# Kernel optimization log

Measured on AMD Instinct MI355X. Metric: run time of the kernel, lower is better.

The kernel has to match this reference:

```python
import jax, jax.numpy as jnp
import numpy as np

DIM = 768
HEADS = 12

def setup_inputs() -> dict:
    key = jax.random.key(0)
    ks = jax.random.split(key, 5)
    x = jax.random.normal(ks[0], (8, 1024, DIM), dtype=jnp.float32)
    s = 1.0 / np.sqrt(DIM)
    W_qkv = jax.random.normal(ks[1], (DIM, 3 * DIM), dtype=jnp.float32) * s
    b_qkv = jax.random.normal(ks[2], (3 * DIM,), dtype=jnp.float32) * 0.01
    W_proj = jax.random.normal(ks[3], (DIM, DIM), dtype=jnp.float32) * s
    b_proj = jax.random.normal(ks[4], (DIM,), dtype=jnp.float32) * 0.01
    return {"x": x, "W_qkv": W_qkv, "b_qkv": b_qkv, "W_proj": W_proj, "b_proj": b_proj}

def reference(x, W_qkv, b_qkv, W_proj, b_proj):
    B, T, D = x.shape
    H = HEADS
    hd = D // H
    scale = hd ** -0.5
    qkv = x @ W_qkv + b_qkv                      # [B,T,3D]
    qkv = qkv.reshape(B, T, 3, H, hd)
    q, k, v = jnp.moveaxis(qkv, 2, 0)            # each [B,T,H,hd]
    q = jnp.transpose(q, (0, 2, 1, 3))           # [B,H,T,hd]
    k = jnp.transpose(k, (0, 2, 1, 3))
    v = jnp.transpose(v, (0, 2, 1, 3))
    attn = jnp.einsum('bhqd,bhkd->bhqk', q, k) * scale
    attn = jax.nn.softmax(attn, axis=-1)
    y = jnp.einsum('bhqk,bhkd->bhqd', attn, v)   # [B,H,T,hd]
    y = jnp.transpose(y, (0, 2, 1, 3)).reshape(B, T, D)
    return y @ W_proj + b_proj
```

## Files before the change

kernel.cpp:

```cpp
#include <hip/hip_runtime.h>

typedef unsigned short u16;
typedef __attribute__((ext_vector_type(8))) short short8;
typedef __attribute__((ext_vector_type(4))) short short4v;
typedef __attribute__((ext_vector_type(2))) int int2v;
typedef __attribute__((ext_vector_type(4))) float f32x4;

#define DIM   768
#define HEADS 12
#define HD    64
#define BATCH 8
#define SEQ   1024
#define MTOK  (BATCH*SEQ)
#define NQKV  (3*DIM)
#define KP    72
#define EPAD  66
#define PSZ   ((size_t)BATCH*HEADS*SEQ*HD)
#define SCQ   0.1803368801f

__device__ __forceinline__ u16 f2bf(float f) {
  unsigned x = __float_as_uint(f);
  x += 0x7fffu + ((x >> 16) & 1u);
  return (u16)(x >> 16);
}

__device__ __forceinline__ void gload16(const u16* g, u16* l) {
  __builtin_amdgcn_global_load_lds(
      (const __attribute__((address_space(1))) unsigned int*)g,
      (__attribute__((address_space(3))) unsigned int*)l, 16, 0, 0);
}

#define XBLK 6144
#define QTBLK 1728
__global__ void cvt_all_k(const float* __restrict__ x,
                          const float* __restrict__ Wqkv,
                          const float* __restrict__ Wproj,
                          u16* __restrict__ xb, u16* __restrict__ wqkvt,
                          u16* __restrict__ wprojt) {
  __shared__ u16 tile[32][33];
  const int blk = blockIdx.x;
  if (blk < XBLK) {
    const int i = blk * 256 + threadIdx.x;
    float4 f = ((const float4*)x)[i];
    short4v o;
    o.x = (short)f2bf(f.x); o.y = (short)f2bf(f.y);
    o.z = (short)f2bf(f.z); o.w = (short)f2bf(f.w);
    ((short4v*)xb)[i] = o;
    return;
  }
  const float* in; u16* out; int K, N, n0, k0;
  if (blk < XBLK + QTBLK) {
    const int t = blk - XBLK;
    in = Wqkv; out = wqkvt; K = DIM; N = NQKV;
    n0 = (t % (NQKV / 32)) * 32; k0 = (t / (NQKV / 32)) * 32;
  } else {
    const int t = blk - XBLK - QTBLK;
    in = Wproj; out = wprojt; K = DIM; N = DIM;
    n0 = (t % (DIM / 32)) * 32; k0 = (t / (DIM / 32)) * 32;
  }
  const int tx = threadIdx.x & 31, ty = threadIdx.x >> 5;
  #pragma unroll
  for (int i = 0; i < 32; i += 8)
    tile[ty + i][tx] = f2bf(in[(size_t)(k0 + ty + i) * N + n0 + tx]);
  __syncthreads();
  #pragma unroll
  for (int i = 0; i < 32; i += 8)
    out[(size_t)(n0 + ty + i) * K + k0 + tx] = tile[tx][ty + i];
}

__global__ __launch_bounds__(256)
void gemm_qkv(const u16* __restrict__ A, const u16* __restrict__ Bt,
              const float* __restrict__ bias, u16* __restrict__ qkv) {
  __shared__ __align__(16) u16 smem[2 * 16384];
  const int tid = threadIdx.x;
  const int w = tid >> 6, lane = tid & 63;
  const int l15 = lane & 15, quad = lane >> 4;
  const int b_ = blockIdx.x;
  const int xcd = b_ & 7, j = b_ >> 3;
  const int m0 = ((j & 7) * 8 + xcd) * 128;
  const int n0 = (j >> 3) * 128;
  const int wm = (w >> 1) * 64, wn = (w & 1) * 64;

  f32x4 acc[4][4] = {};

  const int srow = tid >> 3;
  const int schunk = (tid & 7) ^ (srow & 7);
  const u16* ga = A  + (size_t)(m0 + srow) * DIM + schunk * 8;
  const u16* gb = Bt + (size_t)(n0 + srow) * DIM + schunk * 8;
  const int ldst = tid * 8;

  auto qstage = [&](int c, int k0) {
    u16* base = smem + c * 16384;
    #pragma unroll
    for (int t = 0; t < 4; ++t) {
      gload16(ga + (size_t)t * 32 * DIM + k0, base + t * 2048 + ldst);
      gload16(gb + (size_t)t * 32 * DIM + k0, base + 8192 + t * 2048 + ldst);
    }
  };

  qstage(0, 0);

  #pragma unroll
  for (int it = 0; it < 12; ++it) {
    const int cur = it & 1;
    if (it < 11) qstage(cur ^ 1, (it + 1) * 64);
    if (it < 11) asm volatile("s_waitcnt vmcnt(8)" ::: "memory");
    else         asm volatile("s_waitcnt vmcnt(0)" ::: "memory");
    __builtin_amdgcn_s_barrier();

    const u16* lA = smem + cur * 16384;
    const u16* lB = lA + 8192;
    const int sx = l15 & 7;
    short8 af[4][2], bfr[4][2];
    #pragma unroll
    for (int kh = 0; kh < 2; ++kh) {
      #pragma unroll
      for (int mt = 0; mt < 4; ++mt)
        af[mt][kh] = *(const short8*)&lA[(wm + mt * 16 + l15) * 64 + (((kh * 4 + quad) ^ sx) * 8)];
      #pragma unroll
      for (int nt = 0; nt < 4; ++nt)
        bfr[nt][kh] = *(const short8*)&lB[(wn + nt * 16 + l15) * 64 + (((kh * 4 + quad) ^ sx) * 8)];
    }

    asm volatile("s_waitcnt lgkmcnt(0)" ::: "memory");
    __builtin_amdgcn_s_barrier();

    #pragma unroll
    for (int kh = 0; kh < 2; ++kh)
      #pragma unroll
      for (int mt = 0; mt < 4; ++mt)
        #pragma unroll
        for (int nt = 0; nt < 4; ++nt)
          acc[mt][nt] = __builtin_amdgcn_mfma_f32_16x16x32_bf16(af[mt][kh], bfr[nt][kh], acc[mt][nt], 0, 0, 0);
  }

  const int bb = m0 >> 10;
  const int tb0 = (m0 & 1023) + wm;
  const int nh = n0 + wn;
  const int part = nh / DIM, idx = nh - part * DIM;
  const int h = idx >> 6;

  float bnl[4];
  #pragma unroll
  for (int nt = 0; nt < 4; ++nt) bnl[nt] = bias[nh + nt * 16 + l15];

  if (part < 2) {
    u16* dstbase = qkv + part * PSZ + ((size_t)(bb * HEADS + h) * SEQ + tb0) * HD;
    const float qsc = (part == 0) ? SCQ : 1.0f;
    const int erow = lane >> 3, ec8 = (lane & 7) * 8;
    #pragma unroll
    for (int mt = 0; mt < 4; ++mt) {
      u16* ep = smem + w * (16 * EPAD) + (mt & 1) * (4 * 16 * EPAD);
      #pragma unroll
      for (int nt = 0; nt < 4; ++nt)
        #pragma unroll
        for (int r = 0; r < 4; ++r)
          ep[(quad * 4 + r) * EPAD + nt * 16 + l15] = f2bf((acc[mt][nt][r] + bnl[nt]) * qsc);
      #pragma unroll
      for (int j2 = 0; j2 < 2; ++j2) {
        const int trow = j2 * 8 + erow;
        short8 vrow = *(const short8*)&ep[trow * EPAD + ec8];
        *(short8*)(dstbase + (size_t)(mt * 16 + trow) * HD + ec8) = vrow;
      }
    }
  } else {
    u16* vrow0 = qkv + 2 * PSZ + (size_t)(bb * HEADS + h) * HD * SEQ;
    #pragma unroll
    for (int nt = 0; nt < 4; ++nt) {
      const int d = nt * 16 + l15;
      u16* trow = vrow0 + (size_t)d * SEQ + tb0 + quad * 4;
      #pragma unroll
      for (int mt = 0; mt < 4; ++mt) {
        short4v pv;
        pv.x = (short)f2bf(acc[mt][nt][0] + bnl[nt]);
        pv.y = (short)f2bf(acc[mt][nt][1] + bnl[nt]);
        pv.z = (short)f2bf(acc[mt][nt][2] + bnl[nt]);
        pv.w = (short)f2bf(acc[mt][nt][3] + bnl[nt]);
        *(short4v*)(trow + mt * 16) = pv;
      }
    }
  }
}

__global__ __launch_bounds__(256)
void gemm_proj(const u16* __restrict__ A, const u16* __restrict__ Bt,
               const float* __restrict__ bias, float* __restrict__ outF) {
  __shared__ __align__(16) u16 smem[8 * 128 * 32];
  const int w = threadIdx.x >> 6, lane = threadIdx.x & 63;
  const int l15 = lane & 15, quad = lane >> 4;
  const int b_ = blockIdx.x;
  const int xcd = b_ & 7, j = b_ >> 3;
  const int m0 = ((j & 7) * 8 + xcd) * 128;
  const int n0 = (j >> 3) * 128;
  const int wm = (w >> 1) * 64, wn = (w & 1) * 64;

  f32x4 acc[4][4] = {};

  const int ar = threadIdx.x >> 2, ak = (threadIdx.x & 3) * 8;
  const u16* ga = A  + (size_t)(m0 + ar) * DIM + ak;
  const u16* gb = Bt + (size_t)(n0 + ar) * DIM + ak;
  const int lo = threadIdx.x * 8;

  auto pstage = [&](int c, int k0) {
    u16* base = smem + c * 16384;
    #pragma unroll
    for (int t = 0; t < 2; ++t) {
      gload16(ga + (size_t)t * 64 * DIM + k0,      base + lo + t * 2048);
      gload16(ga + (size_t)t * 64 * DIM + k0 + 32, base + 4096  + lo + t * 2048);
      gload16(gb + (size_t)t * 64 * DIM + k0,      base + 8192  + lo + t * 2048);
      gload16(gb + (size_t)t * 64 * DIM + k0 + 32, base + 12288 + lo + t * 2048);
    }
  };

  pstage(0, 0);
  __syncthreads();

  #pragma unroll
  for (int it = 0; it < 12; ++it) {
    const int cur = it & 1;
    if (it < 11) pstage(cur ^ 1, (it + 1) * 64);
    const u16* hb = smem + cur * 16384;
    #pragma unroll
    for (int kh = 0; kh < 2; ++kh) {
      const u16* lAh = hb + kh * 4096;
      const u16* lBh = hb + 8192 + kh * 4096;
      short8 af[4], bfr[4];
      #pragma unroll
      for (int mt = 0; mt < 4; ++mt)
        af[mt] = *(const short8*)&lAh[(wm + mt * 16 + l15) * 32 + quad * 8];
      #pragma unroll
      for (int nt = 0; nt < 4; ++nt)
        bfr[nt] = *(const short8*)&lBh[(wn + nt * 16 + l15) * 32 + quad * 8];
      #pragma unroll
      for (int mt = 0; mt < 4; ++mt)
        #pragma unroll
        for (int nt = 0; nt < 4; ++nt)
          acc[mt][nt] = __builtin_amdgcn_mfma_f32_16x16x32_bf16(af[mt], bfr[nt], acc[mt][nt], 0, 0, 0);
    }
    __syncthreads();
  }

  #pragma unroll
  for (int nt = 0; nt < 4; ++nt) {
    const int n = n0 + wn + nt * 16 + l15;
    const float bn = bias[n];
    #pragma unroll
    for (int mt = 0; mt < 4; ++mt)
      #pragma unroll
      for (int r = 0; r < 4; ++r) {
        const int m = m0 + wm + mt * 16 + quad * 4 + r;
        outF[(size_t)m * DIM + n] = acc[mt][nt][r] + bn;
      }
  }
}

__global__ __launch_bounds__(512, 4)
void attn_k(const u16* __restrict__ qb, const u16* __restrict__ kb,
            const u16* __restrict__ vtb, u16* __restrict__ yb) {
  const int bh = blockIdx.x, qt = blockIdx.y;
  const int tid = threadIdx.x;
  const int w = tid >> 6, lane = tid & 63;
  const int l15 = lane & 15, quad = lane >> 4;
  const int rg = w & 3;
  const int kh = w >> 2;
  const int nt0 = kh * 2;

  __shared__ __align__(16) u16 smem[26624];
  u16* lPq = smem + 16384 + rg * 2304;
  u16* stg = smem + 17408 + rg * 2304;
  float* fo = (float*)smem;

  const u16* qrow = qb + ((size_t)bh * SEQ + qt * 128 + rg * 32 + l15) * HD;
  short8 aq[2][2];
  #pragma unroll
  for (int qg = 0; qg < 2; ++qg) {
    aq[qg][0] = *(const short8*)(qrow + (size_t)qg * 16 * HD + quad * 8);
    aq[qg][1] = *(const short8*)(qrow + (size_t)qg * 16 * HD + 32 + quad * 8);
  }

  f32x4 o[2][4] = {};
  f32x4 sum[2] = {};

  const u16* kcbase = kb + (size_t)bh * SEQ * HD;
  const u16* vbase  = vtb + (size_t)bh * HD * SEQ;

  const int srow = tid >> 3;
  const int schunk = (tid & 7) ^ (srow & 7);
  const u16* kgs = kcbase + (size_t)srow * HD + schunk * 8;
  const u16* vgs = vbase + (size_t)srow * SEQ + schunk * 8;
  const int dst = tid * 8;

  auto stage = [&](int c, int kc) {
    gload16(kgs + kc * 4096, smem + c * 8192 + dst);
    gload16(vgs + kc * 64,   smem + c * 8192 + 4096 + dst);
  };

  short8 ones;
  #pragma unroll
  for (int i = 0; i < 8; ++i) ones[i] = (short)0x3f80;

  stage(0, 0);

  for (int kc = 0; kc < 16; ++kc) {
    const int cur = kc & 1;
    if (kc < 15) stage(cur ^ 1, kc + 1);
    if (kc < 15) asm volatile("s_waitcnt vmcnt(2)" ::: "memory");
    else         asm volatile("s_waitcnt vmcnt(0)" ::: "memory");
    __builtin_amdgcn_s_barrier();

    const u16* lK = smem + cur * 8192;
    const u16* lV = lK + 4096;
    const int sx = l15 & 7;

    short8 akf[2][2];
    #pragma unroll
    for (int i = 0; i < 2; ++i) {
      const int key = (nt0 + i) * 16 + l15;
      akf[i][0] = *(const short8*)&lK[key * 64 + ((quad ^ sx) * 8)];
      akf[i][1] = *(const short8*)&lK[key * 64 + (((4 + quad) ^ sx) * 8)];
    }

    #pragma unroll
    for (int qg = 0; qg < 2; ++qg) {
      f32x4 s0 = {}, s1 = {};
      __builtin_amdgcn_s_setprio(1);
      s0 = __builtin_amdgcn_mfma_f32_16x16x32_bf16(akf[0][0], aq[qg][0], s0, 0, 0, 0);
      s0 = __builtin_amdgcn_mfma_f32_16x16x32_bf16(akf[0][1], aq[qg][1], s0, 0, 0, 0);
      s1 = __builtin_amdgcn_mfma_f32_16x16x32_bf16(akf[1][0], aq[qg][0], s1, 0, 0, 0);
      s1 = __builtin_amdgcn_mfma_f32_16x16x32_bf16(akf[1][1], aq[qg][1], s1, 0, 0, 0);
      __builtin_amdgcn_s_setprio(0);
      #pragma unroll
      for (int i = 0; i < 2; ++i) {
        const f32x4 s = i ? s1 : s0;
        float p0 = __builtin_amdgcn_exp2f(s[0]);
        float p1 = __builtin_amdgcn_exp2f(s[1]);
        float p2 = __builtin_amdgcn_exp2f(s[2]);
        float p3 = __builtin_amdgcn_exp2f(s[3]);
        int2v pkk;
        pkk.x = (int)__builtin_amdgcn_perm(__float_as_uint(p1), __float_as_uint(p0), 0x07060302u);
        pkk.y = (int)__builtin_amdgcn_perm(__float_as_uint(p3), __float_as_uint(p2), 0x07060302u);
        *(int2v*)&lPq[(qg * 16 + l15) * KP + (nt0 + i) * 16 + quad * 4] = pkk;
      }
    }

    short8 bv[4];
    #pragma unroll
    for (int ntd = 0; ntd < 4; ++ntd)
      bv[ntd] = *(const short8*)&lV[(ntd * 16 + l15) * 64 + (((kh * 4 + quad) ^ sx) * 8)];

    #pragma unroll
    for (int qg = 0; qg < 2; ++qg) {
      const short8 ap = *(const short8*)&lPq[(qg * 16 + l15) * KP + kh * 32 + quad * 8];
      __builtin_amdgcn_s_setprio(1);
      #pragma unroll
      for (int ntd = 0; ntd < 4; ++ntd)
        o[qg][ntd] = __builtin_amdgcn_mfma_f32_16x16x32_bf16(ap, bv[ntd], o[qg][ntd], 0, 0, 0);
      sum[qg] = __builtin_amdgcn_mfma_f32_16x16x32_bf16(ap, ones, sum[qg], 0, 0, 0);
      __builtin_amdgcn_s_setprio(0);
    }

    asm volatile("s_waitcnt lgkmcnt(0)" ::: "memory");
    __builtin_amdgcn_s_barrier();
  }

  if (kh == 1) {
    #pragma unroll
    for (int qg = 0; qg < 2; ++qg)
      #pragma unroll
      for (int r = 0; r < 4; ++r) {
        const int row = rg * 32 + qg * 16 + quad * 4 + r;
        #pragma unroll
        for (int ntd = 0; ntd < 4; ++ntd)
          fo[row * 68 + ntd * 16 + l15] = o[qg][ntd][r];
        if (l15 == 0) fo[row * 68 + 64] = sum[qg][r];
      }
  }
  __syncthreads();

  if (kh == 0) {
    const int b = bh / HEADS, h = bh % HEADS;
    #pragma unroll
    for (int qg = 0; qg < 2; ++qg)
      #pragma unroll
      for (int r = 0; r < 4; ++r) {
        const int lrow = qg * 16 + quad * 4 + r;
        const int row = rg * 32 + lrow;
        const float s = sum[qg][r] + fo[row * 68 + 64];
        const float inv = 1.0f / s;
        #pragma unroll
        for (int ntd = 0; ntd < 4; ++ntd) {
          const float v = (o[qg][ntd][r] + fo[row * 68 + ntd * 16 + l15]) * inv;
          stg[lrow * KP + ntd * 16 + l15] = f2bf(v);
        }
      }
    u16* dst2 = yb + ((size_t)b * SEQ + qt * 128 + rg * 32) * DIM + h * HD;
    const int erow = lane >> 3, ec8 = (lane & 7) * 8;
    #pragma unroll
    for (int j = 0; j < 4; ++j) {
      const int trow = j * 8 + erow;
      short8 vrow = *(const short8*)&stg[trow * KP + ec8];
      *(short8*)(dst2 + (size_t)trow * DIM + ec8) = vrow;
    }
  }
}

extern "C" void kernel_launch(void* const* d_in, const int* in_sizes, int n_in,
                              void* d_out, int out_size, void* d_ws, size_t ws_size,
                              hipStream_t stream) {
  const float* x     = (const float*)d_in[0];
  const float* Wqkv  = (const float*)d_in[1];
  const float* bqkv  = (const float*)d_in[2];
  const float* Wproj = (const float*)d_in[3];
  const float* bproj = (const float*)d_in[4];
  float* out = (float*)d_out;

  u16* xb     = (u16*)d_ws;
  u16* wqkvt  = xb + (size_t)MTOK * DIM;
  u16* wprojt = wqkvt + (size_t)NQKV * DIM;
  u16* qkv_b  = wprojt + (size_t)DIM * DIM;
  u16* y_b    = qkv_b + 3 * PSZ;

  cvt_all_k<<<XBLK + QTBLK + (DIM / 32) * (DIM / 32), 256, 0, stream>>>(
      x, Wqkv, Wproj, xb, wqkvt, wprojt);

  gemm_qkv<<<1152, 256, 0, stream>>>(xb, wqkvt, bqkv, qkv_b);

  attn_k<<<dim3(BATCH * HEADS, SEQ / 128), 512, 0, stream>>>(
      qkv_b, qkv_b + PSZ, qkv_b + 2 * PSZ, y_b);

  gemm_proj<<<384, 256, 0, stream>>>(y_b, wprojt, bproj, out);
}
```

Before: 180.1 us.

## Swizzle proj GEMM LDS layout and use vmcnt-based double-buffer barriers

Reworks the projection GEMM's shared-memory staging so each row holds 64 contiguous k-elements in an XOR-swizzled chunk order, with fragment reads un-swizzled. This targets LDS bank conflicts on the 16-byte fragment loads. The loop now waits with s_waitcnt vmcnt so only the previous stage must land, then barriers, loads all fragments to registers, and barriers again before the MFMAs. The aim is to overlap the next stage's global loads with compute. The result depends on gload16 being an async direct-to-LDS load tracked by vmcnt, and it adds one extra barrier per iteration.

```diff
diff --git a/kernel.cpp b/kernel.cpp
--- a/kernel.cpp
+++ b/kernel.cpp
@@ -185,8 +185,9 @@
 __global__ __launch_bounds__(256)
 void gemm_proj(const u16* __restrict__ A, const u16* __restrict__ Bt,
                const float* __restrict__ bias, float* __restrict__ outF) {
-  __shared__ __align__(16) u16 smem[8 * 128 * 32];
-  const int w = threadIdx.x >> 6, lane = threadIdx.x & 63;
+  __shared__ __align__(16) u16 smem[2 * 16384];
+  const int tid = threadIdx.x;
+  const int w = tid >> 6, lane = tid & 63;
   const int l15 = lane & 15, quad = lane >> 4;
   const int b_ = blockIdx.x;
   const int xcd = b_ & 7, j = b_ >> 3;
@@ -196,48 +197,55 @@
 
   f32x4 acc[4][4] = {};
 
-  const int ar = threadIdx.x >> 2, ak = (threadIdx.x & 3) * 8;
-  const u16* ga = A  + (size_t)(m0 + ar) * DIM + ak;
-  const u16* gb = Bt + (size_t)(n0 + ar) * DIM + ak;
-  const int lo = threadIdx.x * 8;
+  const int srow = tid >> 3;
+  const int schunk = (tid & 7) ^ (srow & 7);
+  const u16* ga = A  + (size_t)(m0 + srow) * DIM + schunk * 8;
+  const u16* gb = Bt + (size_t)(n0 + srow) * DIM + schunk * 8;
+  const int ldst = tid * 8;
 
   auto pstage = [&](int c, int k0) {
     u16* base = smem + c * 16384;
     #pragma unroll
-    for (int t = 0; t < 2; ++t) {
-      gload16(ga + (size_t)t * 64 * DIM + k0,      base + lo + t * 2048);
-      gload16(ga + (size_t)t * 64 * DIM + k0 + 32, base + 4096  + lo + t * 2048);
-      gload16(gb + (size_t)t * 64 * DIM + k0,      base + 8192  + lo + t * 2048);
-      gload16(gb + (size_t)t * 64 * DIM + k0 + 32, base + 12288 + lo + t * 2048);
+    for (int t = 0; t < 4; ++t) {
+      gload16(ga + (size_t)t * 32 * DIM + k0, base + t * 2048 + ldst);
+      gload16(gb + (size_t)t * 32 * DIM + k0, base + 8192 + t * 2048 + ldst);
     }
   };
 
   pstage(0, 0);
-  __syncthreads();
 
   #pragma unroll
   for (int it = 0; it < 12; ++it) {
     const int cur = it & 1;
     if (it < 11) pstage(cur ^ 1, (it + 1) * 64);
-    const u16* hb = smem + cur * 16384;
+    if (it < 11) asm volatile("s_waitcnt vmcnt(8)" ::: "memory");
+    else         asm volatile("s_waitcnt vmcnt(0)" ::: "memory");
+    __builtin_amdgcn_s_barrier();
+
+    const u16* lA = smem + cur * 16384;
+    const u16* lB = lA + 8192;
+    const int sx = l15 & 7;
+    short8 af[4][2], bfr[4][2];
     #pragma unroll
     for (int kh = 0; kh < 2; ++kh) {
-      const u16* lAh = hb + kh * 4096;
-      const u16* lBh = hb + 8192 + kh * 4096;
-      short8 af[4], bfr[4];
       #pragma unroll
       for (int mt = 0; mt < 4; ++mt)
-        af[mt] = *(const short8*)&lAh[(wm + mt * 16 + l15) * 32 + quad * 8];
+        af[mt][kh] = *(const short8*)&lA[(wm + mt * 16 + l15) * 64 + (((kh * 4 + quad) ^ sx) * 8)];
       #pragma unroll
       for (int nt = 0; nt < 4; ++nt)
-        bfr[nt] = *(const short8*)&lBh[(wn + nt * 16 + l15) * 32 + quad * 8];
+        bfr[nt][kh] = *(const short8*)&lB[(wn + nt * 16 + l15) * 64 + (((kh * 4 + quad) ^ sx) * 8)];
+    }
+
+    asm volatile("s_waitcnt lgkmcnt(0)" ::: "memory");
+    __builtin_amdgcn_s_barrier();
+
+    #pragma unroll
+    for (int kh = 0; kh < 2; ++kh)
       #pragma unroll
       for (int mt = 0; mt < 4; ++mt)
         #pragma unroll
         for (int nt = 0; nt < 4; ++nt)
-          acc[mt][nt] = __builtin_amdgcn_mfma_f32_16x16x32_bf16(af[mt], bfr[nt], acc[mt][nt], 0, 0, 0);
-    }
-    __syncthreads();
+          acc[mt][nt] = __builtin_amdgcn_mfma_f32_16x16x32_bf16(af[mt][kh], bfr[nt][kh], acc[mt][nt], 0, 0, 0);
   }
 
   #pragma unroll
```

Result: no change. 180.7 us (+0.4%).
